# Kernel optimization log

Hardware: AMD Instinct MI355X
Metric: run time of the kernel (lower is better)

## Reference

```python
import jax, jax.numpy as jnp
import numpy as np

B, TD, TE, V, D, DFF, L, H = 16, 256, 1024, 5000, 512, 2048, 6, 8

def setup_inputs():
    key = jax.random.key(0)
    ks = jax.random.split(key, 32)
    s = 0.02
    def w(k, shape):
        return jax.random.normal(k, shape, jnp.float32) * s
    # targets drawn in [3, V) so the eos filter in the torch code is a no-op
    inp = {
        "targets": jax.random.randint(ks[0], (B, TD), 3, V),
        "target_lengths": jax.random.randint(ks[1], (B,), TD // 2, TD + 1),
        "encoder_outputs": jax.random.normal(ks[2], (B, TE, D), jnp.float32),
        "encoder_output_lengths": jax.random.randint(ks[3], (B,), TE // 2, TE + 1),
        "emb": w(ks[4], (V, D)),
        "W_in": w(ks[5], (D, D)), "b_in": jnp.zeros((D,), jnp.float32),
        "ln1_g": jnp.ones((L, D), jnp.float32), "ln1_b": jnp.zeros((L, D), jnp.float32),
        "Wq1": w(ks[6], (L, D, D)), "bq1": jnp.zeros((L, D), jnp.float32),
        "Wk1": w(ks[7], (L, D, D)), "bk1": jnp.zeros((L, D), jnp.float32),
        "Wv1": w(ks[8], (L, D, D)), "bv1": jnp.zeros((L, D), jnp.float32),
        "Wo1": w(ks[9], (L, D, D)), "bo1": jnp.zeros((L, D), jnp.float32),
        "ln2_g": jnp.ones((L, D), jnp.float32), "ln2_b": jnp.zeros((L, D), jnp.float32),
        "Wq2": w(ks[10], (L, D, D)), "bq2": jnp.zeros((L, D), jnp.float32),
        "Wk2": w(ks[11], (L, D, D)), "bk2": jnp.zeros((L, D), jnp.float32),
        "Wv2": w(ks[12], (L, D, D)), "bv2": jnp.zeros((L, D), jnp.float32),
        "Wo2": w(ks[13], (L, D, D)), "bo2": jnp.zeros((L, D), jnp.float32),
        "ln3_g": jnp.ones((L, D), jnp.float32), "ln3_b": jnp.zeros((L, D), jnp.float32),
        "W_ff1": w(ks[14], (L, D, DFF)), "b_ff1": jnp.zeros((L, DFF), jnp.float32),
        "W_ff2": w(ks[15], (L, DFF, D)), "b_ff2": jnp.zeros((L, D), jnp.float32),
    }
    return inp

def _ln(x, g, b, eps=1e-5):
    m = x.mean(-1, keepdims=True)
    v = ((x - m) ** 2).mean(-1, keepdims=True)
    return (x - m) * jax.lax.rsqrt(v + eps) * g + b

def _mha(q, k, v, Wq, bq, Wk, bk, Wv, bv, Wo, bo, mask):
    Bq, Tq, Dm = q.shape
    dh = Dm // H
    def heads(x, W, bias):
        y = x @ W + bias
        return y.reshape(x.shape[0], x.shape[1], H, dh).transpose(0, 2, 1, 3)  # (B,H,T,dh)
    qh, kh, vh = heads(q, Wq, bq), heads(k, Wk, bk), heads(v, Wv, bv)
    sc = jnp.einsum('bhqd,bhkd->bhqk', qh, kh) / jnp.sqrt(jnp.float32(dh))
    sc = jnp.where(mask[:, None, :, :], jnp.float32(-1e9), sc)
    a = jax.nn.softmax(sc, axis=-1)
    ctx = jnp.einsum('bhqk,bhkd->bhqd', a, vh).transpose(0, 2, 1, 3).reshape(Bq, Tq, Dm)
    return ctx @ Wo + bo

def _pos_encoding(length, dim):
    pos = jnp.arange(length, dtype=jnp.float32)[:, None]
    div = jnp.exp(jnp.arange(0, dim, 2, dtype=jnp.float32) * (-jnp.log(jnp.float32(10000.0)) / dim))
    pe = jnp.zeros((length, dim), jnp.float32)
    pe = pe.at[:, 0::2].set(jnp.sin(pos * div)).at[:, 1::2].set(jnp.cos(pos * div))
    return pe

def _forward(targets, target_lengths, encoder_output_lengths, encoder_outputs, emb, W_in, b_in, ln1_g, ln1_b, Wq1, bq1, Wk1, bk1, Wv1, bv1, Wo1, bo1, ln2_g, ln2_b, Wq2, bq2, Wk2, bk2, Wv2, bv2, Wo2, bo2, ln3_g, ln3_b, W_ff1, b_ff1, W_ff2, b_ff2):
    Bsz, Td = targets.shape
    Te = encoder_outputs.shape[1]
    key_pad = jnp.arange(Td)[None, :] >= target_lengths[:, None]            # (B, Td) pad keys
    causal = jnp.triu(jnp.ones((Td, Td), bool), k=1)                        # subsequent mask
    self_mask = key_pad[:, None, :] | causal[None]                          # (B, Td, Td)
    enc_pad = jnp.arange(Te)[None, :] >= encoder_output_lengths[:, None]    # (B, Te)
    enc_mask = jnp.broadcast_to(enc_pad[:, None, :], (Bsz, Td, Te))
    # TransformerEmbedding: lookup * sqrt(dim), then sinusoidal PE, then input_proj
    x = emb[targets] * jnp.sqrt(jnp.float32(D)) + _pos_encoding(Td, D)[None]
    x = x @ W_in + b_in
    for l in range(L):  # pre-LN decoder layers: self-attn, cross-attn, FFN
        h = _ln(x, ln1_g[l], ln1_b[l])
        x = x + _mha(h, h, h, Wq1[l], bq1[l], Wk1[l], bk1[l], Wv1[l], bv1[l], Wo1[l], bo1[l], self_mask)
        h = _ln(x, ln2_g[l], ln2_b[l])
        x = x + _mha(h, encoder_outputs, encoder_outputs, Wq2[l], bq2[l], Wk2[l], bk2[l], Wv2[l], bv2[l], Wo2[l], bo2[l], enc_mask)
        h = _ln(x, ln3_g[l], ln3_b[l])
        x = x + (jax.nn.relu(h @ W_ff1[l] + b_ff1[l]) @ W_ff2[l] + b_ff2[l])
    # torch code stacks step_outputs[:, di, :] over di, i.e. returns the hidden states (B, Td, D)
    return x

def reference(targets, target_lengths, encoder_outputs, encoder_output_lengths, emb, W_in, b_in, ln1_g, ln1_b, Wq1, bq1, Wk1, bk1, Wv1, bv1, Wo1, bo1, ln2_g, ln2_b, Wq2, bq2, Wk2, bk2, Wv2, bv2, Wo2, bo2, ln3_g, ln3_b, W_ff1, b_ff1, W_ff2, b_ff2):
    return _forward(targets, target_lengths, encoder_output_lengths, encoder_outputs, emb, W_in, b_in, ln1_g, ln1_b, Wq1, bq1, Wk1, bk1, Wv1, bv1, Wo1, bo1, ln2_g, ln2_b, Wq2, bq2, Wk2, bk2, Wv2, bv2, Wo2, bo2, ln3_g, ln3_b, W_ff1, b_ff1, W_ff2, b_ff2)
```

## Files before the change

### kernel.cpp

```cpp
#include <hip/hip_runtime.h>
#include <hip/hip_bf16.h>

#define BB   16
#define TD   256
#define TE   1024
#define DM   512
#define DFF  2048
#define NL   6
#define NH   8
#define DH   64

typedef unsigned short u16;
typedef unsigned int u32;
typedef short short8 __attribute__((ext_vector_type(8)));
typedef float f32x4 __attribute__((ext_vector_type(4)));

__device__ __forceinline__ float b2f(u16 u) {
    unsigned int x = ((unsigned int)u) << 16;
    float f;
    __builtin_memcpy(&f, &x, 4);
    return f;
}
__device__ __forceinline__ u16 f2b(float f) {
    unsigned int x;
    __builtin_memcpy(&x, &f, 4);
    unsigned int r = x + 0x7fffu + ((x >> 16) & 1u);
    return (u16)(r >> 16);
}

__device__ __forceinline__ void gload_lds16(const u16* g, u16* l) {
    __builtin_amdgcn_global_load_lds(
        (const __attribute__((address_space(1))) unsigned int*)g,
        (__attribute__((address_space(3))) unsigned int*)l, 16, 0, 0);
}

__global__ __launch_bounds__(256) void cvt_kernel(const float* __restrict__ in,
                                                  u16* __restrict__ out, int n4) {
    int i = blockIdx.x * 256 + threadIdx.x;
    if (i < n4) {
        float4 v = reinterpret_cast<const float4*>(in)[i];
        ushort4 o;
        o.x = f2b(v.x); o.y = f2b(v.y); o.z = f2b(v.z); o.w = f2b(v.w);
        reinterpret_cast<ushort4*>(out)[i] = o;
    }
}

template <int NMAT>
struct PtrArr { const float* p[NMAT]; };

template <int NMAT>
__global__ __launch_bounds__(256) void tr_kernel(PtrArr<NMAT> P, u16* __restrict__ out,
                                                 int K, int N) {
    __shared__ u16 t[64][65];
    const float* W = P.p[blockIdx.z];
    u16* O = out + (size_t)blockIdx.z * K * N;
    int n0 = blockIdx.x * 64, k0 = blockIdx.y * 64;
    int tid = threadIdx.x;
    int r = tid >> 4, c = (tid & 15) * 4;
#pragma unroll
    for (int p = 0; p < 4; ++p) {
        int k = r + p * 16;
        float4 v = *reinterpret_cast<const float4*>(&W[(size_t)(k0 + k) * N + n0 + c]);
        t[c + 0][k] = f2b(v.x);
        t[c + 1][k] = f2b(v.y);
        t[c + 2][k] = f2b(v.z);
        t[c + 3][k] = f2b(v.w);
    }
    __syncthreads();
#pragma unroll
    for (int p = 0; p < 4; ++p) {
        int n = r + p * 16;
        ushort4 o;
        o.x = t[n][c]; o.y = t[n][c + 1]; o.z = t[n][c + 2]; o.w = t[n][c + 3];
        *reinterpret_cast<ushort4*>(&O[(size_t)(n0 + n) * K + k0 + c]) = o;
    }
}

__global__ __launch_bounds__(256) void embed_kernel(const int* __restrict__ targets,
                                                    const float* __restrict__ emb,
                                                    u16* __restrict__ out) {
    int row = blockIdx.x;
    int t   = row & (TD - 1);
    int tgt = targets[row];
    const float c = -0.017988946039015984f;
    for (int d = threadIdx.x; d < DM; d += 256) {
        float e   = emb[(size_t)tgt * DM + d] * 22.627416997969522f;
        int   i2  = d & ~1;
        float div = expf(c * (float)i2);
        float arg = (float)t * div;
        float pe  = (d & 1) ? cosf(arg) : sinf(arg);
        out[(size_t)row * DM + d] = f2b(e + pe);
    }
}

__global__ __launch_bounds__(256) void ln_kernel(const float* __restrict__ X,
                                                 const float* __restrict__ g,
                                                 const float* __restrict__ b,
                                                 size_t vo,
                                                 u16* __restrict__ O) {
    int row = blockIdx.x;
    int tid = threadIdx.x;
    float2 v = *reinterpret_cast<const float2*>(&X[(size_t)row * DM + 2 * tid]);
    float s  = v.x + v.y;
    float sq = v.x * v.x + v.y * v.y;
    __shared__ float red[8];
    int lane = tid & 63, wid = tid >> 6;
#pragma unroll
    for (int off = 32; off; off >>= 1) {
        s  += __shfl_xor(s, off);
        sq += __shfl_xor(sq, off);
    }
    if (lane == 0) { red[wid] = s; red[wid + 4] = sq; }
    __syncthreads();
    float mean = (red[0] + red[1] + red[2] + red[3]) * (1.0f / 512.0f);
    float ex2  = (red[4] + red[5] + red[6] + red[7]) * (1.0f / 512.0f);
    float var  = ex2 - mean * mean;
    float rs   = rsqrtf(var + 1e-5f);
    float o0 = (v.x - mean) * rs * g[vo + 2 * tid]     + b[vo + 2 * tid];
    float o1 = (v.y - mean) * rs * g[vo + 2 * tid + 1] + b[vo + 2 * tid + 1];
    u32 w = (u32)f2b(o0) | ((u32)f2b(o1) << 16);
    reinterpret_cast<u32*>(O)[(size_t)row * (DM / 2) + tid] = w;
}

template <int TM, int TN, bool OUTBF, bool RELU, bool RES>
__global__ __launch_bounds__(256) void gemm_bt(const u16* __restrict__ A,
                                               const u16* __restrict__ Bt,
                                               const float* __restrict__ bias, size_t bofs,
                                               const float* __restrict__ resid,
                                               void* __restrict__ C,
                                               int M, int N, int K) {
    __shared__ u16 As[2][TM * 32];
    __shared__ u16 Bs[2][TN * 32];
    int tid = threadIdx.x, wave = tid >> 6, lane = tid & 63;
    int col0 = blockIdx.x * TN, row0 = blockIdx.y * TM;
    constexpr int WM = TM / 2, WN = TN / 2;
    int wm = (wave >> 1) * WM, wn = (wave & 1) * WN;
    int lq = lane >> 4, lc = lane & 15;
    constexpr int NI = WM / 16, NJ = WN / 16;
    f32x4 acc[NI][NJ] = {};
    int srow = lane >> 2;
    int scol = (lane & 3) * 8;

    auto stage = [&](int buf, int k0) {
#pragma unroll
        for (int s = 0; s < TM / 64; ++s) {
            int rbase = wave * (TM / 4) + s * 16;
            gload_lds16(A + (size_t)(row0 + rbase + srow) * K + k0 + scol, &As[buf][rbase * 32]);
        }
#pragma unroll
        for (int s = 0; s < TN / 64; ++s) {
            int rbase = wave * (TN / 4) + s * 16;
            gload_lds16(Bt + (size_t)(col0 + rbase + srow) * K + k0 + scol, &Bs[buf][rbase * 32]);
        }
    };

    stage(0, 0);
    __syncthreads();
    int cur = 0;
    for (int k0 = 0; k0 < K; k0 += 32) {
        if (k0 + 32 < K) stage(cur ^ 1, k0 + 32);
        short8 af[NI], bf[NJ];
#pragma unroll
        for (int i = 0; i < NI; ++i)
            af[i] = *reinterpret_cast<const short8*>(&As[cur][(wm + i * 16 + lc) * 32 + lq * 8]);
#pragma unroll
        for (int j = 0; j < NJ; ++j)
            bf[j] = *reinterpret_cast<const short8*>(&Bs[cur][(wn + j * 16 + lc) * 32 + lq * 8]);
#pragma unroll
        for (int i = 0; i < NI; ++i)
#pragma unroll
            for (int j = 0; j < NJ; ++j)
                acc[i][j] = __builtin_amdgcn_mfma_f32_16x16x32_bf16(af[i], bf[j], acc[i][j], 0, 0, 0);
        __syncthreads();
        cur ^= 1;
    }

#pragma unroll
    for (int j = 0; j < NJ; ++j) {
        int n = col0 + wn + j * 16 + lc;
        float bv = bias[bofs + n];
#pragma unroll
        for (int i = 0; i < NI; ++i) {
#pragma unroll
            for (int r = 0; r < 4; ++r) {
                int m = row0 + wm + i * 16 + lq * 4 + r;
                float v = acc[i][j][r] + bv;
                if (RES)  v += resid[(size_t)m * N + n];
                if (RELU) v = fmaxf(v, 0.0f);
                if (OUTBF) ((u16*)C)[(size_t)m * N + n] = f2b(v);
                else       ((float*)C)[(size_t)m * N + n] = v;
            }
        }
    }
}

template <int NG>
struct MGrp {
    const u16* A[NG];
    u16* out[NG];
    const float* bias[NG];
    int mlim[NG];
    int skip[NG];
};

template <int TM, int TN, int NG>
__global__ __launch_bounds__(256) void gemm_bt_multi(MGrp<NG> mg,
                                                     const u16* __restrict__ Bt,
                                                     int K,
                                                     const int* __restrict__ lens,
                                                     int rbShift) {
    __shared__ u16 As[2][TM * 32];
    __shared__ u16 Bs[2][TN * 32];
    int tid = threadIdx.x, wave = tid >> 6, lane = tid & 63;
    int col0 = blockIdx.x * TN, row0 = blockIdx.y * TM;
    int g  = col0 >> 9;
    int c0 = col0 & 511;

    if (row0 >= mg.mlim[g]) return;
    if (mg.skip[g]) {
        int bb  = row0 >> rbShift;
        int rl  = row0 & ((1 << rbShift) - 1);
        int lim = (lens[bb] + 63) & ~63;
        if (rl >= lim) return;
    }
    const u16* A = mg.A[g];

    constexpr int WM = TM / 2, WN = TN / 2;
    int wm = (wave >> 1) * WM, wn = (wave & 1) * WN;
    int lq = lane >> 4, lc = lane & 15;
    constexpr int NI = WM / 16, NJ = WN / 16;
    f32x4 acc[NI][NJ] = {};
    int srow = lane >> 2;
    int scol = (lane & 3) * 8;

    auto stage = [&](int buf, int k0) {
#pragma unroll
        for (int s = 0; s < TM / 64; ++s) {
            int rbase = wave * (TM / 4) + s * 16;
            gload_lds16(A + (size_t)(row0 + rbase + srow) * K + k0 + scol, &As[buf][rbase * 32]);
        }
#pragma unroll
        for (int s = 0; s < TN / 64; ++s) {
            int rbase = wave * (TN / 4) + s * 16;
            gload_lds16(Bt + (size_t)(col0 + rbase + srow) * K + k0 + scol, &Bs[buf][rbase * 32]);
        }
    };

    stage(0, 0);
    __syncthreads();
    int cur = 0;
    for (int k0 = 0; k0 < K; k0 += 32) {
        if (k0 + 32 < K) stage(cur ^ 1, k0 + 32);
        short8 af[NI], bf[NJ];
#pragma unroll
        for (int i = 0; i < NI; ++i)
            af[i] = *reinterpret_cast<const short8*>(&As[cur][(wm + i * 16 + lc) * 32 + lq * 8]);
#pragma unroll
        for (int j = 0; j < NJ; ++j)
            bf[j] = *reinterpret_cast<const short8*>(&Bs[cur][(wn + j * 16 + lc) * 32 + lq * 8]);
#pragma unroll
        for (int i = 0; i < NI; ++i)
#pragma unroll
            for (int j = 0; j < NJ; ++j)
                acc[i][j] = __builtin_amdgcn_mfma_f32_16x16x32_bf16(af[i], bf[j], acc[i][j], 0, 0, 0);
        __syncthreads();
        cur ^= 1;
    }

    u16* O = mg.out[g];
    const float* bp = mg.bias[g];
#pragma unroll
    for (int j = 0; j < NJ; ++j) {
        int n = c0 + wn + j * 16 + lc;
        float bv = bp[n];
#pragma unroll
        for (int i = 0; i < NI; ++i) {
#pragma unroll
            for (int r = 0; r < 4; ++r) {
                int m = row0 + wm + i * 16 + lq * 4 + r;
                O[(size_t)m * 512 + n] = f2b(acc[i][j][r] + bv);
            }
        }
    }
}

#define QSTR 72

__device__ __forceinline__ int vidx(int d, int kp) {
    return d * 32 + (kp ^ (((d >> 2) & 7) << 2));
}

__global__ __launch_bounds__(256) void fattn_mfma(const u16* __restrict__ Q,
                                                  const u16* __restrict__ K,
                                                  const u16* __restrict__ V,
                                                  const int* __restrict__ lens,
                                                  u16* __restrict__ O,
                                                  int Tq, int Tk, int causal) {
    __shared__ u16 Qs[64 * QSTR];
    __shared__ u16 Ks[2][64 * QSTR];
    __shared__ u16 Ps[64 * QSTR];
    __shared__ u32 Vs32[2][64 * 32];
    int tid  = threadIdx.x;
    int wg      = blockIdx.x;
    int chunk   = gridDim.x >> 3;
    int logical = (wg & 7) * chunk + (wg >> 3);
    int nq   = Tq / 64;
    int b    = logical / (NH * nq);
    int rem  = logical - b * (NH * nq);
    int h    = rem / nq;
    int qt0  = (rem - h * nq) * 64;
    int len  = lens[b];
    int wave = tid >> 6, lane = tid & 63;
    int lq = lane >> 4, lc = lane & 15;
    int sr = tid >> 4;
    int sd = (tid & 15) * 4;

    short8 bones;
    {
        u16 v = (lc == 0) ? (u16)0x3F80 : (u16)0;
        u16 tmp[8] = { v, v, v, v, v, v, v, v };
        __builtin_memcpy(&bones, tmp, 16);
    }

#pragma unroll
    for (int i = 0; i < 4; ++i) {
        int q = sr + i * 16;
        ushort4 v = *reinterpret_cast<const ushort4*>(
            &Q[(size_t)(b * Tq + qt0 + q) * DM + h * DH + sd]);
        ushort4 w;
        w.x = f2b(b2f(v.x) * 0.125f); w.y = f2b(b2f(v.y) * 0.125f);
        w.z = f2b(b2f(v.z) * 0.125f); w.w = f2b(b2f(v.w) * 0.125f);
        *reinterpret_cast<ushort4*>(&Qs[q * QSTR + sd]) = w;
    }

    ushort4 kr[4], vr[2][2];
#pragma unroll
    for (int i = 0; i < 4; ++i) {
        int k = sr + i * 16;
        kr[i] = *reinterpret_cast<const ushort4*>(&K[(size_t)(b * Tk + k) * DM + h * DH + sd]);
    }
#pragma unroll
    for (int i = 0; i < 2; ++i) {
        int kp = sr + i * 16;
#pragma unroll
        for (int p = 0; p < 2; ++p)
            vr[i][p] = *reinterpret_cast<const ushort4*>(
                &V[(size_t)(b * Tk + 2 * kp + p) * DM + h * DH + sd]);
    }
#pragma unroll
    for (int i = 0; i < 4; ++i) {
        int k = sr + i * 16;
        *reinterpret_cast<ushort4*>(&Ks[0][k * QSTR + sd]) = kr[i];
    }
#pragma unroll
    for (int i = 0; i < 2; ++i) {
        int kp = sr + i * 16;
        u16 a0[4], a1[4];
        __builtin_memcpy(a0, &vr[i][0], 8);
        __builtin_memcpy(a1, &vr[i][1], 8);
#pragma unroll
        for (int j = 0; j < 4; ++j)
            Vs32[0][vidx(sd + j, kp)] = (u32)a0[j] | ((u32)a1[j] << 16);
    }
    __syncthreads();

    short8 aq0 = *reinterpret_cast<const short8*>(&Qs[(wave * 16 + lc) * QSTR + lq * 8]);
    short8 aq1 = *reinterpret_cast<const short8*>(&Qs[(wave * 16 + lc) * QSTR + 32 + lq * 8]);

    f32x4 Ow[4] = {};
    f32x4 Ol = {};

    int kend = causal ? min(len, qt0 + 64) : len;
    int cur = 0;
    for (int kt0 = 0; kt0 < kend; kt0 += 64) {
        bool more = (kt0 + 64) < kend;
        if (more) {
#pragma unroll
            for (int i = 0; i < 4; ++i) {
                int k = kt0 + 64 + sr + i * 16;
                kr[i] = *reinterpret_cast<const ushort4*>(
                    &K[(size_t)(b * Tk + k) * DM + h * DH + sd]);
            }
#pragma unroll
            for (int i = 0; i < 2; ++i) {
                int kp = sr + i * 16;
#pragma unroll
                for (int p = 0; p < 2; ++p)
                    vr[i][p] = *reinterpret_cast<const ushort4*>(
                        &V[(size_t)(b * Tk + kt0 + 64 + 2 * kp + p) * DM + h * DH + sd]);
            }
        }

        f32x4 sa[4] = {};
        __builtin_amdgcn_s_setprio(1);
#pragma unroll
        for (int n = 0; n < 4; ++n) {
            short8 bk0 = *reinterpret_cast<const short8*>(&Ks[cur][(n * 16 + lc) * QSTR + lq * 8]);
            short8 bk1 = *reinterpret_cast<const short8*>(&Ks[cur][(n * 16 + lc) * QSTR + 32 + lq * 8]);
            sa[n] = __builtin_amdgcn_mfma_f32_16x16x32_bf16(aq0, bk0, sa[n], 0, 0, 0);
            sa[n] = __builtin_amdgcn_mfma_f32_16x16x32_bf16(aq1, bk1, sa[n], 0, 0, 0);
        }
        __builtin_amdgcn_s_setprio(0);

        int qrow_base = qt0 + wave * 16 + lq * 4;
        bool nomask = (kt0 + 64 <= len) &&
                      (!causal || (kt0 + 63 <= qt0 + wave * 16));
        if (nomask) {
#pragma unroll
            for (int r = 0; r < 4; ++r)
#pragma unroll
                for (int n = 0; n < 4; ++n)
                    Ps[(wave * 16 + lq * 4 + r) * QSTR + n * 16 + lc] =
                        f2b(__expf(sa[n][r] - 8.0f));
        } else {
#pragma unroll
            for (int r = 0; r < 4; ++r) {
                int qrow = qrow_base + r;
#pragma unroll
                for (int n = 0; n < 4; ++n) {
                    int key = kt0 + n * 16 + lc;
                    bool inv = (key >= len) || (causal && key > qrow);
                    float p = inv ? 0.0f : __expf(sa[n][r] - 8.0f);
                    Ps[(wave * 16 + lq * 4 + r) * QSTR + n * 16 + lc] = f2b(p);
                }
            }
        }

        short8 ap0 = *reinterpret_cast<const short8*>(&Ps[(wave * 16 + lc) * QSTR + lq * 8]);
        short8 ap1 = *reinterpret_cast<const short8*>(&Ps[(wave * 16 + lc) * QSTR + 32 + lq * 8]);
        __builtin_amdgcn_s_setprio(1);
#pragma unroll
        for (int n = 0; n < 4; ++n) {
            int d = n * 16 + lc;
#pragma unroll
            for (int ks = 0; ks < 2; ++ks) {
                int base = d * 32 + ((ks * 16 + lq * 4) ^ (((d >> 2) & 7) << 2));
                uint4 vv = *reinterpret_cast<const uint4*>(&Vs32[cur][base]);
                short8 bv;
                __builtin_memcpy(&bv, &vv, 16);
                Ow[n] = __builtin_amdgcn_mfma_f32_16x16x32_bf16(ks ? ap1 : ap0, bv, Ow[n], 0, 0, 0);
            }
        }
        Ol = __builtin_amdgcn_mfma_f32_16x16x32_bf16(ap0, bones, Ol, 0, 0, 0);
        Ol = __builtin_amdgcn_mfma_f32_16x16x32_bf16(ap1, bones, Ol, 0, 0, 0);
        __builtin_amdgcn_s_setprio(0);

        if (more) {
#pragma unroll
            for (int i = 0; i < 4; ++i) {
                int k = sr + i * 16;
                *reinterpret_cast<ushort4*>(&Ks[cur ^ 1][k * QSTR + sd]) = kr[i];
            }
#pragma unroll
            for (int i = 0; i < 2; ++i) {
                int kp = sr + i * 16;
                u16 a0[4], a1[4];
                __builtin_memcpy(a0, &vr[i][0], 8);
                __builtin_memcpy(a1, &vr[i][1], 8);
#pragma unroll
                for (int j = 0; j < 4; ++j)
                    Vs32[cur ^ 1][vidx(sd + j, kp)] = (u32)a0[j] | ((u32)a1[j] << 16);
            }
            __syncthreads();
            cur ^= 1;
        }
    }

#pragma unroll
    for (int r = 0; r < 4; ++r) {
        float lsum = __shfl(Ol[r], lane & 48);
        float inv = 1.0f / lsum;
        size_t rowoff = (size_t)(b * Tq + qt0 + wave * 16 + lq * 4 + r) * DM + h * DH;
#pragma unroll
        for (int n = 0; n < 4; ++n)
            O[rowoff + n * 16 + lc] = f2b(Ow[n][r] * inv);
    }
}

extern "C" void kernel_launch(void* const* d_in, const int* in_sizes, int n_in,
                              void* d_out, int out_size, void* d_ws, size_t ws_size,
                              hipStream_t stream) {
    const int*   targets = (const int*)d_in[0];
    const int*   tlen    = (const int*)d_in[1];
    const float* enc     = (const float*)d_in[2];
    const int*   elen    = (const int*)d_in[3];
    const float* emb     = (const float*)d_in[4];
    const float* W_in    = (const float*)d_in[5];
    const float* b_in    = (const float*)d_in[6];
    const float* ln1_g   = (const float*)d_in[7];
    const float* ln1_b   = (const float*)d_in[8];
    const float* Wq1 = (const float*)d_in[9],  *bq1 = (const float*)d_in[10];
    const float* Wk1 = (const float*)d_in[11], *bk1 = (const float*)d_in[12];
    const float* Wv1 = (const float*)d_in[13], *bv1 = (const float*)d_in[14];
    const float* Wo1 = (const float*)d_in[15], *bo1 = (const float*)d_in[16];
    const float* ln2_g = (const float*)d_in[17], *ln2_b = (const float*)d_in[18];
    const float* Wq2 = (const float*)d_in[19], *bq2 = (const float*)d_in[20];
    const float* Wk2 = (const float*)d_in[21], *bk2 = (const float*)d_in[22];
    const float* Wv2 = (const float*)d_in[23], *bv2 = (const float*)d_in[24];
    const float* Wo2 = (const float*)d_in[25], *bo2 = (const float*)d_in[26];
    const float* ln3_g = (const float*)d_in[27], *ln3_b = (const float*)d_in[28];
    const float* W_ff1 = (const float*)d_in[29], *b_ff1 = (const float*)d_in[30];
    const float* W_ff2 = (const float*)d_in[31], *b_ff2 = (const float*)d_in[32];

    float* ws   = (float*)d_ws;
    float* x    = ws;
    u16*   hb   = (u16*)(ws + 2097152);
    u16*   qb   = (u16*)(ws + 3145728);
    u16*   ctx  = (u16*)(ws + 4194304);
    u16*   kb   = (u16*)(ws + 5242880);
    u16*   vb   = (u16*)(ws + 9437184);
    u16*   encb = (u16*)(ws + 13631488);
    u16*   wt_dm = (u16*)(ws + 17825792);
    u16*   wt_f1 = (u16*)(ws + 24248320);
    u16*   wt_f2 = (u16*)(ws + 27394048);
    u16*   ffh  = kb;

    PtrArr<49> pdm;
    pdm.p[0] = W_in;
    for (int l = 0; l < NL; ++l) {
        const float* ws8[8] = { Wq1, Wk1, Wv1, Wo1, Wq2, Wk2, Wv2, Wo2 };
        for (int j = 0; j < 8; ++j) pdm.p[1 + l * 8 + j] = ws8[j] + (size_t)l * DM * DM;
    }
    PtrArr<6> pf1, pf2;
    for (int l = 0; l < NL; ++l) {
        pf1.p[l] = W_ff1 + (size_t)l * DM * DFF;
        pf2.p[l] = W_ff2 + (size_t)l * DFF * DM;
    }
    tr_kernel<49><<<dim3(8, 8, 49), 256, 0, stream>>>(pdm, wt_dm, 512, 512);
    tr_kernel<6><<<dim3(32, 8, 6), 256, 0, stream>>>(pf1, wt_f1, 512, 2048);
    tr_kernel<6><<<dim3(8, 32, 6), 256, 0, stream>>>(pf2, wt_f2, 2048, 512);

    const size_t WDM = (size_t)512 * 512;
    const size_t WFF = (size_t)512 * 2048;

    const dim3 gdm(8, 64);
    const dim3 gqkv(24, 64);
    const dim3 gq2kv(12, 128);
    const dim3 gf1(16, 32);
    const dim3 gattn(BB * NH * (TD / 64));

    cvt_kernel<<<8192, 256, 0, stream>>>(enc, encb, BB * TE * DM / 4);
    embed_kernel<<<4096, 256, 0, stream>>>(targets, emb, hb);
    gemm_bt<64, 64, false, false, false><<<gdm, 256, 0, stream>>>(hb, wt_dm, b_in, 0, nullptr, x, 4096, 512, 512);

    for (int l = 0; l < NL; ++l) {
        const size_t vo = (size_t)l * DM;
        const size_t fv = (size_t)l * DFF;
        const u16* tq1 = wt_dm + (1 + l * 8 + 0) * WDM;
        const u16* to1 = wt_dm + (1 + l * 8 + 3) * WDM;
        const u16* tq2 = wt_dm + (1 + l * 8 + 4) * WDM;
        const u16* to2 = wt_dm + (1 + l * 8 + 7) * WDM;
        const u16* tf1 = wt_f1 + l * WFF;
        const u16* tf2 = wt_f2 + l * WFF;
        const bool last = (l == NL - 1);

        ln_kernel<<<4096, 256, 0, stream>>>(x, ln1_g, ln1_b, vo, hb);
        {
            MGrp<3> mg;
            mg.A[0] = hb;  mg.A[1] = hb;  mg.A[2] = hb;
            mg.out[0] = qb; mg.out[1] = kb; mg.out[2] = vb;
            mg.bias[0] = bq1 + vo; mg.bias[1] = bk1 + vo; mg.bias[2] = bv1 + vo;
            mg.mlim[0] = 4096; mg.mlim[1] = 4096; mg.mlim[2] = 4096;
            mg.skip[0] = 0; mg.skip[1] = 1; mg.skip[2] = 1;
            gemm_bt_multi<64, 64, 3><<<gqkv, 256, 0, stream>>>(mg, tq1, 512, tlen, 8);
        }
        fattn_mfma<<<gattn, 256, 0, stream>>>(qb, kb, vb, tlen, ctx, TD, TD, 1);
        gemm_bt<64, 64, false, false, true><<<gdm, 256, 0, stream>>>(ctx, to1, bo1, vo, x, x, 4096, 512, 512);

        ln_kernel<<<4096, 256, 0, stream>>>(x, ln2_g, ln2_b, vo, hb);
        {
            MGrp<3> mg;
            mg.A[0] = hb;  mg.A[1] = encb; mg.A[2] = encb;
            mg.out[0] = qb; mg.out[1] = kb; mg.out[2] = vb;
            mg.bias[0] = bq2 + vo; mg.bias[1] = bk2 + vo; mg.bias[2] = bv2 + vo;
            mg.mlim[0] = 4096; mg.mlim[1] = 16384; mg.mlim[2] = 16384;
            mg.skip[0] = 0; mg.skip[1] = 1; mg.skip[2] = 1;
            gemm_bt_multi<128, 128, 3><<<gq2kv, 256, 0, stream>>>(mg, tq2, 512, elen, 10);
        }
        fattn_mfma<<<gattn, 256, 0, stream>>>(qb, kb, vb, elen, ctx, TD, TE, 0);
        gemm_bt<64, 64, false, false, true><<<gdm, 256, 0, stream>>>(ctx, to2, bo2, vo, x, x, 4096, 512, 512);

        ln_kernel<<<4096, 256, 0, stream>>>(x, ln3_g, ln3_b, vo, hb);
        gemm_bt<128, 128, true, true, false><<<gf1, 256, 0, stream>>>(hb, tf1, b_ff1, fv, nullptr, ffh, 4096, 2048, 512);
        gemm_bt<64, 64, false, false, true><<<gdm, 256, 0, stream>>>(
            ffh, tf2, b_ff2, vo, x, last ? (float*)d_out : x, 4096, 512, 2048);
    }
}
```

Baseline: 1.267 ms.

## Fuse LayerNorm into the A-operand staging of the following GEMMs

Removes the three standalone LayerNorm kernels per layer. Each consuming GEMM (QKV, cross-attn Q, FF1) now computes per-row mean and rstd in a prologue, then normalizes fp32 x to bf16 while staging A tiles into LDS. This saves 18 launches and the bf16 write and re-read of the normalized activations. In exchange, stats are recomputed by every column block, A staging becomes synchronous register loads instead of async global-to-LDS, and the fp32 A reads double the A traffic.

```diff
diff --git a/kernel.cpp b/kernel.cpp
--- a/kernel.cpp
+++ b/kernel.cpp
@@ -93,37 +93,69 @@
     }
 }
 
-__global__ __launch_bounds__(256) void ln_kernel(const float* __restrict__ X,
-                                                 const float* __restrict__ g,
-                                                 const float* __restrict__ b,
-                                                 size_t vo,
-                                                 u16* __restrict__ O) {
-    int row = blockIdx.x;
-    int tid = threadIdx.x;
-    float2 v = *reinterpret_cast<const float2*>(&X[(size_t)row * DM + 2 * tid]);
-    float s  = v.x + v.y;
-    float sq = v.x * v.x + v.y * v.y;
-    __shared__ float red[8];
-    int lane = tid & 63, wid = tid >> 6;
-#pragma unroll
-    for (int off = 32; off; off >>= 1) {
+template <int TM>
+__device__ __forceinline__ void ln_stats(const float* __restrict__ Xf, int row0,
+                                         float* sm_mean, float* sm_rstd, int tid) {
+    constexpr int TPR = 256 / TM;
+    constexpr int EPT = DM / TPR;
+    int lrow = tid / TPR, lseg = tid % TPR;
+    const float* xr = Xf + (size_t)(row0 + lrow) * DM + lseg * EPT;
+    float s = 0.f, sq = 0.f;
+#pragma unroll 8
+    for (int j = 0; j < EPT; j += 4) {
+        float4 v = *reinterpret_cast<const float4*>(&xr[j]);
+        s  += v.x + v.y + v.z + v.w;
+        sq += v.x * v.x + v.y * v.y + v.z * v.z + v.w * v.w;
+    }
+#pragma unroll
+    for (int off = 1; off < TPR; off <<= 1) {
         s  += __shfl_xor(s, off);
         sq += __shfl_xor(sq, off);
     }
-    if (lane == 0) { red[wid] = s; red[wid + 4] = sq; }
+    if (lseg == 0) {
+        float mean = s * (1.0f / 512.0f);
+        float var  = sq * (1.0f / 512.0f) - mean * mean;
+        sm_mean[lrow] = mean;
+        sm_rstd[lrow] = rsqrtf(var + 1e-5f);
+    }
     __syncthreads();
-    float mean = (red[0] + red[1] + red[2] + red[3]) * (1.0f / 512.0f);
-    float ex2  = (red[4] + red[5] + red[6] + red[7]) * (1.0f / 512.0f);
-    float var  = ex2 - mean * mean;
-    float rs   = rsqrtf(var + 1e-5f);
-    float o0 = (v.x - mean) * rs * g[vo + 2 * tid]     + b[vo + 2 * tid];
-    float o1 = (v.y - mean) * rs * g[vo + 2 * tid + 1] + b[vo + 2 * tid + 1];
-    u32 w = (u32)f2b(o0) | ((u32)f2b(o1) << 16);
-    reinterpret_cast<u32*>(O)[(size_t)row * (DM / 2) + tid] = w;
-}
-
-template <int TM, int TN, bool OUTBF, bool RELU, bool RES>
+}
+
+template <int TM>
+__device__ __forceinline__ void stage_ln(const float* __restrict__ Xf,
+                                         const float* __restrict__ lng,
+                                         const float* __restrict__ lnb, size_t vo,
+                                         int row0, int k0, u16* As,
+                                         const float* sm_mean, const float* sm_rstd,
+                                         int wave, int srow, int scol) {
+#pragma unroll
+    for (int s = 0; s < TM / 64; ++s) {
+        int rbase = wave * (TM / 4) + s * 16;
+        int row   = rbase + srow;
+        float mean = sm_mean[row], rstd = sm_rstd[row];
+        const float* xp = Xf + (size_t)(row0 + row) * DM + k0 + scol;
+        float4 va = *reinterpret_cast<const float4*>(xp);
+        float4 vb = *reinterpret_cast<const float4*>(xp + 4);
+        const float* gp = lng + vo + k0 + scol;
+        const float* bp = lnb + vo + k0 + scol;
+        u16 t[8];
+        t[0] = f2b((va.x - mean) * rstd * gp[0] + bp[0]);
+        t[1] = f2b((va.y - mean) * rstd * gp[1] + bp[1]);
+        t[2] = f2b((va.z - mean) * rstd * gp[2] + bp[2]);
+        t[3] = f2b((va.w - mean) * rstd * gp[3] + bp[3]);
+        t[4] = f2b((vb.x - mean) * rstd * gp[4] + bp[4]);
+        t[5] = f2b((vb.y - mean) * rstd * gp[5] + bp[5]);
+        t[6] = f2b((vb.z - mean) * rstd * gp[6] + bp[6]);
+        t[7] = f2b((vb.w - mean) * rstd * gp[7] + bp[7]);
+        __builtin_memcpy(&As[(size_t)(rbase + srow) * 32 + scol], t, 16);
+    }
+}
+
+template <int TM, int TN, bool OUTBF, bool RELU, bool RES, bool LNA>
 __global__ __launch_bounds__(256) void gemm_bt(const u16* __restrict__ A,
+                                               const float* __restrict__ Xf,
+                                               const float* __restrict__ lng,
+                                               const float* __restrict__ lnb, size_t vo,
                                                const u16* __restrict__ Bt,
                                                const float* __restrict__ bias, size_t bofs,
                                                const float* __restrict__ resid,
@@ -131,6 +163,7 @@
                                                int M, int N, int K) {
     __shared__ u16 As[2][TM * 32];
     __shared__ u16 Bs[2][TN * 32];
+    __shared__ float sm_mean[TM], sm_rstd[TM];
     int tid = threadIdx.x, wave = tid >> 6, lane = tid & 63;
     int col0 = blockIdx.x * TN, row0 = blockIdx.y * TM;
     constexpr int WM = TM / 2, WN = TN / 2;
@@ -141,11 +174,18 @@
     int srow = lane >> 2;
     int scol = (lane & 3) * 8;
 
+    if (LNA) ln_stats<TM>(Xf, row0, sm_mean, sm_rstd, tid);
+
     auto stage = [&](int buf, int k0) {
-#pragma unroll
-        for (int s = 0; s < TM / 64; ++s) {
-            int rbase = wave * (TM / 4) + s * 16;
-            gload_lds16(A + (size_t)(row0 + rbase + srow) * K + k0 + scol, &As[buf][rbase * 32]);
+        if (LNA) {
+            stage_ln<TM>(Xf, lng, lnb, vo, row0, k0, As[buf], sm_mean, sm_rstd,
+                         wave, srow, scol);
+        } else {
+#pragma unroll
+            for (int s = 0; s < TM / 64; ++s) {
+                int rbase = wave * (TM / 4) + s * 16;
+                gload_lds16(A + (size_t)(row0 + rbase + srow) * K + k0 + scol, &As[buf][rbase * 32]);
+            }
         }
 #pragma unroll
         for (int s = 0; s < TN / 64; ++s) {
@@ -203,14 +243,18 @@
     int skip[NG];
 };
 
-template <int TM, int TN, int NG>
+template <int TM, int TN, int NG, int LNMODE>
 __global__ __launch_bounds__(256) void gemm_bt_multi(MGrp<NG> mg,
+                                                     const float* __restrict__ Xf,
+                                                     const float* __restrict__ lng,
+                                                     const float* __restrict__ lnb, size_t vo,
                                                      const u16* __restrict__ Bt,
                                                      int K,
                                                      const int* __restrict__ lens,
                                                      int rbShift) {
     __shared__ u16 As[2][TM * 32];
     __shared__ u16 Bs[2][TN * 32];
+    __shared__ float sm_mean[TM], sm_rstd[TM];
     int tid = threadIdx.x, wave = tid >> 6, lane = tid & 63;
     int col0 = blockIdx.x * TN, row0 = blockIdx.y * TM;
     int g  = col0 >> 9;
@@ -224,6 +268,7 @@
         if (rl >= lim) return;
     }
     const u16* A = mg.A[g];
+    bool useln = (LNMODE == 2) || (LNMODE == 1 && g == 0);
 
     constexpr int WM = TM / 2, WN = TN / 2;
     int wm = (wave >> 1) * WM, wn = (wave & 1) * WN;
@@ -233,11 +278,18 @@
     int srow = lane >> 2;
     int scol = (lane & 3) * 8;
 
+    if (LNMODE && useln) ln_stats<TM>(Xf, row0, sm_mean, sm_rstd, tid);
+
     auto stage = [&](int buf, int k0) {
-#pragma unroll
-        for (int s = 0; s < TM / 64; ++s) {
-            int rbase = wave * (TM / 4) + s * 16;
-            gload_lds16(A + (size_t)(row0 + rbase + srow) * K + k0 + scol, &As[buf][rbase * 32]);
+        if (LNMODE && useln) {
+            stage_ln<TM>(Xf, lng, lnb, vo, row0, k0, As[buf], sm_mean, sm_rstd,
+                         wave, srow, scol);
+        } else {
+#pragma unroll
+            for (int s = 0; s < TM / 64; ++s) {
+                int rbase = wave * (TM / 4) + s * 16;
+                gload_lds16(A + (size_t)(row0 + rbase + srow) * K + k0 + scol, &As[buf][rbase * 32]);
+            }
         }
 #pragma unroll
         for (int s = 0; s < TN / 64; ++s) {
@@ -541,7 +593,8 @@
 
     cvt_kernel<<<8192, 256, 0, stream>>>(enc, encb, BB * TE * DM / 4);
     embed_kernel<<<4096, 256, 0, stream>>>(targets, emb, hb);
-    gemm_bt<64, 64, false, false, false><<<gdm, 256, 0, stream>>>(hb, wt_dm, b_in, 0, nullptr, x, 4096, 512, 512);
+    gemm_bt<64, 64, false, false, false, false><<<gdm, 256, 0, stream>>>(
+        hb, nullptr, nullptr, nullptr, 0, wt_dm, b_in, 0, nullptr, x, 4096, 512, 512);
 
     for (int l = 0; l < NL; ++l) {
         const size_t vo = (size_t)l * DM;
@@ -554,7 +607,6 @@
         const u16* tf2 = wt_f2 + l * WFF;
         const bool last = (l == NL - 1);
 
-        ln_kernel<<<4096, 256, 0, stream>>>(x, ln1_g, ln1_b, vo, hb);
         {
             MGrp<3> mg;
             mg.A[0] = hb;  mg.A[1] = hb;  mg.A[2] = hb;
@@ -562,12 +614,13 @@
             mg.bias[0] = bq1 + vo; mg.bias[1] = bk1 + vo; mg.bias[2] = bv1 + vo;
             mg.mlim[0] = 4096; mg.mlim[1] = 4096; mg.mlim[2] = 4096;
             mg.skip[0] = 0; mg.skip[1] = 1; mg.skip[2] = 1;
-            gemm_bt_multi<64, 64, 3><<<gqkv, 256, 0, stream>>>(mg, tq1, 512, tlen, 8);
+            gemm_bt_multi<64, 64, 3, 2><<<gqkv, 256, 0, stream>>>(
+                mg, x, ln1_g, ln1_b, vo, tq1, 512, tlen, 8);
         }
         fattn_mfma<<<gattn, 256, 0, stream>>>(qb, kb, vb, tlen, ctx, TD, TD, 1);
-        gemm_bt<64, 64, false, false, true><<<gdm, 256, 0, stream>>>(ctx, to1, bo1, vo, x, x, 4096, 512, 512);
-
-        ln_kernel<<<4096, 256, 0, stream>>>(x, ln2_g, ln2_b, vo, hb);
+        gemm_bt<64, 64, false, false, true, false><<<gdm, 256, 0, stream>>>(
+            ctx, nullptr, nullptr, nullptr, 0, to1, bo1, vo, x, x, 4096, 512, 512);
+
         {
             MGrp<3> mg;
             mg.A[0] = hb;  mg.A[1] = encb; mg.A[2] = encb;
@@ -575,14 +628,17 @@
             mg.bias[0] = bq2 + vo; mg.bias[1] = bk2 + vo; mg.bias[2] = bv2 + vo;
             mg.mlim[0] = 4096; mg.mlim[1] = 16384; mg.mlim[2] = 16384;
             mg.skip[0] = 0; mg.skip[1] = 1; mg.skip[2] = 1;
-            gemm_bt_multi<128, 128, 3><<<gq2kv, 256, 0, stream>>>(mg, tq2, 512, elen, 10);
+            gemm_bt_multi<128, 128, 3, 1><<<gq2kv, 256, 0, stream>>>(
+                mg, x, ln2_g, ln2_b, vo, tq2, 512, elen, 10);
         }
         fattn_mfma<<<gattn, 256, 0, stream>>>(qb, kb, vb, elen, ctx, TD, TE, 0);
-        gemm_bt<64, 64, false, false, true><<<gdm, 256, 0, stream>>>(ctx, to2, bo2, vo, x, x, 4096, 512, 512);
-
-        ln_kernel<<<4096, 256, 0, stream>>>(x, ln3_g, ln3_b, vo, hb);
-        gemm_bt<128, 128, true, true, false><<<gf1, 256, 0, stream>>>(hb, tf1, b_ff1, fv, nullptr, ffh, 4096, 2048, 512);
-        gemm_bt<64, 64, false, false, true><<<gdm, 256, 0, stream>>>(
-            ffh, tf2, b_ff2, vo, x, last ? (float*)d_out : x, 4096, 512, 2048);
-    }
-}
+        gemm_bt<64, 64, false, false, true, false><<<gdm, 256, 0, stream>>>(
+            ctx, nullptr, nullptr, nullptr, 0, to2, bo2, vo, x, x, 4096, 512, 512);
+
+        gemm_bt<128, 128, true, true, false, true><<<gf1, 256, 0, stream>>>(
+            nullptr, x, ln3_g, ln3_b, vo, tf1, b_ff1, fv, nullptr, ffh, 4096, 2048, 512);
+        gemm_bt<64, 64, false, false, true, false><<<gdm, 256, 0, stream>>>(
+            ffh, nullptr, nullptr, nullptr, 0, tf2, b_ff2, vo, x,
+            last ? (float*)d_out : x, 4096, 512, 2048);
+    }
+}
```

Result: slower. 1.593 ms (+25.7%).
